# Kernel tuning notes

Hardware: AMD Instinct MI355X
Metric: run time of the kernel (lower is better)

Reference implementation:

```python
import jax, jax.numpy as jnp
from jax import lax
import numpy as np

STRIDE = 16
FH, FW, FC = 100, 160, 256
IMG_H, IMG_W = FH * STRIDE, FW * STRIDE
MIN_SIZE = 16.0
PRE_NMS, POST_NMS = 6000, 300
NMS_T, OUT_NMS_T, SCORE_T = 0.7, 0.5, 0.5
NC = 21          # classes incl. background
POOL, MPOOL = 7, 14
HID = 1024
MC = 128         # mask head channels


def box_iou(a, b):
    # a: [N,4], b: [M,4] in (x1,y1,x2,y2)
    area_a = (a[:, 2] - a[:, 0]) * (a[:, 3] - a[:, 1])
    area_b = (b[:, 2] - b[:, 0]) * (b[:, 3] - b[:, 1])
    lt = jnp.maximum(a[:, None, :2], b[None, :, :2])
    rb = jnp.minimum(a[:, None, 2:], b[None, :, 2:])
    wh = jnp.clip(rb - lt, 0.0)
    inter = wh[..., 0] * wh[..., 1]
    return inter / (area_a[:, None] + area_b[None, :] - inter + 1e-9)


def greedy_nms(iou, thresh):
    # boxes assumed sorted by score desc; returns boolean keep mask
    n = iou.shape[0]
    idxs = jnp.arange(n)
    def body(i, keep):
        sup = keep[i] & (iou[i] > thresh) & (idxs > i)
        return keep & ~sup
    return lax.fori_loop(0, n, body, jnp.ones((n,), bool))


def decode_boxes(deltas, boxes):
    # deltas [...,4], boxes broadcastable [...,4]
    w = boxes[..., 2] - boxes[..., 0]
    h = boxes[..., 3] - boxes[..., 1]
    cx = boxes[..., 0] + 0.5 * w
    cy = boxes[..., 1] + 0.5 * h
    dx, dy, dw, dh = deltas[..., 0], deltas[..., 1], deltas[..., 2], deltas[..., 3]
    pcx = dx * w + cx
    pcy = dy * h + cy
    pw = w * jnp.exp(jnp.minimum(dw, 4.0))
    ph = h * jnp.exp(jnp.minimum(dh, 4.0))
    return jnp.stack([pcx - 0.5 * pw, pcy - 0.5 * ph, pcx + 0.5 * pw, pcy + 0.5 * ph], axis=-1)


def clip_boxes(b):
    return jnp.stack([
        jnp.clip(b[..., 0], 0.0, IMG_W), jnp.clip(b[..., 1], 0.0, IMG_H),
        jnp.clip(b[..., 2], 0.0, IMG_W), jnp.clip(b[..., 3], 0.0, IMG_H)], axis=-1)


def roi_align(feat, rois, out):
    # feat [C,H,W], rois [R,4] in feature-map coords; 1 bilinear sample per bin center
    C, H, W = feat.shape
    R = rois.shape[0]
    x1, y1, x2, y2 = rois[:, 0], rois[:, 1], rois[:, 2], rois[:, 3]
    bw = (x2 - x1) / out
    bh = (y2 - y1) / out
    ctr = jnp.arange(out, dtype=feat.dtype) + 0.5
    sx = x1[:, None] + ctr[None, :] * bw[:, None] - 0.5   # [R,out]
    sy = y1[:, None] + ctr[None, :] * bh[:, None] - 0.5
    xx = jnp.broadcast_to(sx[:, None, :], (R, out, out))
    yy = jnp.broadcast_to(sy[:, :, None], (R, out, out))
    x0 = jnp.clip(jnp.floor(xx), 0, W - 2)
    y0 = jnp.clip(jnp.floor(yy), 0, H - 2)
    fx = jnp.clip(xx - x0, 0.0, 1.0)
    fy = jnp.clip(yy - y0, 0.0, 1.0)
    x0i, y0i = x0.astype(jnp.int32), y0.astype(jnp.int32)
    v00 = feat[:, y0i, x0i]        # [C,R,out,out]
    v01 = feat[:, y0i, x0i + 1]
    v10 = feat[:, y0i + 1, x0i]
    v11 = feat[:, y0i + 1, x0i + 1]
    o = (v00 * ((1 - fy) * (1 - fx))[None] + v01 * ((1 - fy) * fx)[None]
         + v10 * (fy * (1 - fx))[None] + v11 * (fy * fx)[None])
    return o.transpose(1, 0, 2, 3)  # [R,C,out,out]


def setup_inputs() -> dict:
    key = jax.random.key(0)
    ks = jax.random.split(key, 12)
    A = FH * FW * 9
    features = jax.random.normal(ks[0], (1, FC, FH, FW), jnp.float32)
    rpn_logits = jax.random.normal(ks[1], (A, 2), jnp.float32)
    rpn_deltas = jax.random.normal(ks[2], (A, 4), jnp.float32) * 0.1
    # anchor grid: 3 scales x 3 ratios at every stride-16 cell
    cx = (np.arange(FW) + 0.5) * STRIDE
    cy = (np.arange(FH) + 0.5) * STRIDE
    cyg, cxg = np.meshgrid(cy, cx, indexing='ij')  # [FH,FW]
    ws, hs = [], []
    for s in (64.0, 128.0, 256.0):
        for r in (0.5, 1.0, 2.0):
            ws.append(s * np.sqrt(r)); hs.append(s / np.sqrt(r))
    ws = np.asarray(ws, np.float32); hs = np.asarray(hs, np.float32)
    anc = np.stack([cxg[..., None] - ws / 2, cyg[..., None] - hs / 2,
                    cxg[..., None] + ws / 2, cyg[..., None] + hs / 2], axis=-1)
    anchors = jnp.asarray(anc.reshape(-1, 4), jnp.float32)
    W1 = jax.random.normal(ks[3], (FC * POOL * POOL, HID), jnp.float32) * 0.02
    b1 = jnp.zeros((HID,), jnp.float32)
    Wc = jax.random.normal(ks[4], (HID, NC), jnp.float32) * 0.02
    bc = jnp.zeros((NC,), jnp.float32)
    Wr = jax.random.normal(ks[5], (HID, NC * 4), jnp.float32) * 0.02
    br = jnp.zeros((NC * 4,), jnp.float32)
    mw1 = jax.random.normal(ks[6], (MC, FC, 3, 3), jnp.float32) * 0.02
    mb1 = jnp.zeros((MC,), jnp.float32)
    mwd = jax.random.normal(ks[7], (MC, MC, 2, 2), jnp.float32) * 0.02
    mbd = jnp.zeros((MC,), jnp.float32)
    mwo = jax.random.normal(ks[8], (NC, MC, 1, 1), jnp.float32) * 0.02
    mbo = jnp.zeros((NC,), jnp.float32)
    return dict(features=features, rpn_logits=rpn_logits, rpn_deltas=rpn_deltas,
                anchors=anchors, W1=W1, b1=b1, Wc=Wc, bc=bc, Wr=Wr, br=br,
                mw1=mw1, mb1=mb1, mwd=mwd, mbd=mbd, mwo=mwo, mbo=mbo)


def reference(features, rpn_logits, rpn_deltas, anchors, W1, b1, Wc, bc, Wr, br,
              mw1, mb1, mwd, mbd, mwo, mbo):
    feat = features[0]  # [C,FH,FW]
    # --- RPN proposal stage (detached, as in the torch code) ---
    scores = lax.stop_gradient(jax.nn.softmax(rpn_logits, axis=1)[:, 1])
    rois_all = clip_boxes(decode_boxes(lax.stop_gradient(rpn_deltas), anchors))
    ok = ((rois_all[:, 2] - rois_all[:, 0]) >= MIN_SIZE) & ((rois_all[:, 3] - rois_all[:, 1]) >= MIN_SIZE)
    scores = jnp.where(ok, scores, -jnp.inf)
    vals, idx = lax.top_k(scores, PRE_NMS)
    boxes = rois_all[idx]
    keep = greedy_nms(box_iou(boxes, boxes), NMS_T)
    v2, i2 = lax.top_k(jnp.where(keep, vals, -jnp.inf), POST_NMS)
    rois = boxes[i2]  # [R,4]
    # --- ROI heads ---
    roi7 = roi_align(feat, rois / STRIDE, POOL)
    roi14 = roi_align(feat, rois / STRIDE, MPOOL)
    R = POST_NMS
    h = jax.nn.relu(roi7.reshape(R, -1) @ W1 + b1)
    cls_logits = h @ Wc + bc                       # [R,NC]
    roi_deltas = (h @ Wr + br).reshape(R, NC, 4)
    dn = ('NCHW', 'OIHW', 'NCHW')
    x = jax.nn.relu(lax.conv_general_dilated(roi14, mw1, (1, 1), ((1, 1), (1, 1)),
                                             dimension_numbers=dn) + mb1[None, :, None, None])
    x = jax.nn.relu(lax.conv_general_dilated(x, mwd, (1, 1), ((1, 1), (1, 1)), lhs_dilation=(2, 2),
                                             dimension_numbers=dn) + mbd[None, :, None, None])
    mask_logits = lax.conv_general_dilated(x, mwo, (1, 1), ((0, 0), (0, 0)),
                                           dimension_numbers=dn) + mbo[None, :, None, None]  # [R,NC,28,28]
    # --- decode per-class boxes, score/size filter, class-agnostic output NMS ---
    pred_boxes = clip_boxes(decode_boxes(roi_deltas, rois[:, None, :]))  # [R,NC,4]
    sc = jax.nn.softmax(cls_logits, axis=1)[:, 1:].reshape(-1)           # drop background
    bx = pred_boxes[:, 1:].reshape(-1, 4)
    ci = jnp.broadcast_to(jnp.arange(1, NC)[None, :], (R, NC - 1)).reshape(-1) - 1
    ml = mask_logits[:, 1:].reshape(-1, 28, 28)
    valid = (sc > SCORE_T) & ((bx[:, 2] - bx[:, 0]) >= 1.0) & ((bx[:, 3] - bx[:, 1]) >= 1.0)
    scm = jnp.where(valid, sc, -jnp.inf)
    n = scm.shape[0]
    dv, order = lax.top_k(scm, n)     # full descending sort
    dbx = bx[order]
    dci = ci[order]
    dml = ml[order]
    k2 = greedy_nms(box_iou(dbx, dbx), OUT_NMS_T) & jnp.isfinite(dv)
    det_scores = jnp.where(k2, dv, 0.0)
    return det_scores, dbx, dci, k2, dml
```

## Files before the change

kernel.cpp:

```cpp
#include <hip/hip_runtime.h>
#include <stdint.h>

#pragma clang fp contract(off)

typedef unsigned int u32;
typedef unsigned short u16;
typedef unsigned long long u64;
typedef float f32x4 __attribute__((ext_vector_type(4)));
typedef u16 u16x8 __attribute__((ext_vector_type(8)));

#define DEV __device__ __forceinline__

DEV float bf2f(u16 u){ union{u32 i; float f;} v; v.i=((u32)u)<<16; return v.f; }
DEV u16 f2bf(float f){ union{float f; u32 i;} v; v.f=f; u32 b=v.i; return (u16)((b + 0x7fffu + ((b>>16)&1u))>>16); }
DEV u32 fkey(float f){ union{float f; u32 i;} v; v.f=f; u32 b=v.i; return (b&0x80000000u)? ~b : (b|0x80000000u); }
DEV float exp_cr(float x){ return (float)exp((double)x); }

DEV void mfma16(f32x4& d, u16x8 a, u16x8 b){
  asm volatile("v_mfma_f32_16x16x32_bf16 %0, %1, %2, %0" : "+v"(d) : "v"(a), "v"(b));
}

DEV void gload_lds16(const void* g, void* l){
  __builtin_amdgcn_global_load_lds((const __attribute__((address_space(1))) unsigned int*)g,
                                   (__attribute__((address_space(3))) unsigned int*)l, 16, 0, 0);
}

DEV u64 rfl64(u64 v){
  return ((u64)__builtin_amdgcn_readfirstlane((u32)(v>>32))<<32) |
         (u64)__builtin_amdgcn_readfirstlane((u32)v);
}

__global__ void k_rpn(const float* __restrict__ logits, const float* __restrict__ deltas,
                      const float* __restrict__ anchors, float* __restrict__ scores,
                      float* __restrict__ rois_all, u32* __restrict__ hist){
  int i=blockIdx.x*256+threadIdx.x;
  if(i>=144000) return;
  float l0=logits[2*i], l1=logits[2*i+1];
  float m=fmaxf(l0,l1);
  float e0=exp_cr(l0-m), e1=exp_cr(l1-m);
  float s=e1/(e0+e1);
  float a0=anchors[4*i],a1=anchors[4*i+1],a2=anchors[4*i+2],a3=anchors[4*i+3];
  float w=a2-a0, hh=a3-a1;
  float cx=a0+0.5f*w, cy=a1+0.5f*hh;
  float dx=deltas[4*i],dy=deltas[4*i+1],dwv=deltas[4*i+2],dhv=deltas[4*i+3];
  float pcx=dx*w+cx, pcy=dy*hh+cy;
  float pw=w*exp_cr(fminf(dwv,4.f)), ph=hh*exp_cr(fminf(dhv,4.f));
  float x1=fminf(fmaxf(pcx-0.5f*pw,0.f),2560.f);
  float y1=fminf(fmaxf(pcy-0.5f*ph,0.f),1600.f);
  float x2=fminf(fmaxf(pcx+0.5f*pw,0.f),2560.f);
  float y2=fminf(fmaxf(pcy+0.5f*ph,0.f),1600.f);
  float4 bb; bb.x=x1;bb.y=y1;bb.z=x2;bb.w=y2;
  *(float4*)(rois_all+4*i)=bb;
  bool ok=(x2-x1>=16.f)&&(y2-y1>=16.f);
  float sc=ok? s : -INFINITY;
  scores[i]=sc;
  if(ok) atomicAdd(&hist[fkey(sc)>>16],1u);
}

__global__ void k_findbin(const u32* __restrict__ hist, u32* __restrict__ cnt){
  __shared__ u32 cs[1024];
  int t=threadIdx.x;
  u32 s=0;
  for(int b=0;b<64;b++) s+=hist[t*64+b];
  cs[t]=s;
  __syncthreads();
  if(t==0){
    u32 acc=0; int tc=1023;
    for(; tc>=0; tc--){ if(acc+cs[tc]>=6000u) break; acc+=cs[tc]; }
    if(tc<0) tc=0;
    u32 B=(u32)tc*64u;
    for(int b=63;b>=0;b--){
      u32 hb=hist[tc*64+b];
      if(acc+hb>=6000u){ B=(u32)(tc*64+b); break; }
      acc+=hb;
    }
    cnt[2]=B;
  }
}

__global__ void k_compact(const float* __restrict__ scores, u32* __restrict__ cnt, u64* __restrict__ keys){
  int i=blockIdx.x*256+threadIdx.x;
  if(i>=144000) return;
  u32 u=fkey(scores[i]);
  if((u>>16) >= cnt[2]){
    u32 pos=atomicAdd(&cnt[0],1u);
    if(pos<8192u) keys[pos]=((u64)u<<32)|(u64)(~(u32)i);
  }
}

template<bool FROMCNT>
__global__ __launch_bounds__(1024) void k_sort8k(const u64* __restrict__ keys, const u32* __restrict__ cnt,
                                                 int n_fixed, u32* __restrict__ out_idx){
  __shared__ u64 K[8192];
  int n = FROMCNT ? (int)cnt[0] : n_fixed;
  if(n>8192) n=8192;
  for(int i=threadIdx.x;i<8192;i+=1024) K[i]=(i<n)? keys[i] : 0ull;
  __syncthreads();
  for(int k=2;k<=8192;k<<=1){
    for(int j=k>>1;j>0;j>>=1){
      for(int t=threadIdx.x;t<8192;t+=1024){
        int p=t^j;
        if(p>t){
          u64 a=K[t], b=K[p];
          bool up=((t&k)==0);
          if((a<b)==up){ K[t]=b; K[p]=a; }
        }
      }
      __syncthreads();
    }
  }
  for(int i=threadIdx.x;i<6000;i+=1024) out_idx[i]=~((u32)K[i]);
}

__global__ void k_gather6k(const u32* __restrict__ selidx, const float* __restrict__ rois_all,
                           float* __restrict__ boxes6k){
  int i=blockIdx.x*256+threadIdx.x;
  if(i>=6000) return;
  u32 g=selidx[i];
  float4 b=*(const float4*)(rois_all+4*g);
  *(float4*)(boxes6k+4*i)=b;
}

template<int TR>
__global__ void k_masks(const float* __restrict__ boxes, const u32* __restrict__ limitPtr, int limitFixed,
                        float thresh, u64* __restrict__ masks){
  int limit = limitPtr? (int)*limitPtr : limitFixed;
  if(limit>6000) limit=6000;
  long total=(long)limit*94;
  int lane=threadIdx.x&63;
  long w0=(long)blockIdx.x*4 + (threadIdx.x>>6);
  long stride=(long)gridDim.x*4;
  for(long w=w0; w<total; w+=stride){
    int row=(int)(w/94), wrd=(int)(w-(long)row*94);
    int j=wrd*64+lane;
    float4 a=*(const float4*)(boxes+4*row);
    bool bit=false;
    if(j<limit && j>row){
      float4 b=*(const float4*)(boxes+4*j);
      float area_a=(a.z-a.x)*(a.w-a.y);
      float area_b=(b.z-b.x)*(b.w-b.y);
      float ltx=fmaxf(a.x,b.x), lty=fmaxf(a.y,b.y);
      float rbx=fminf(a.z,b.z), rby=fminf(a.w,b.w);
      float wv=fmaxf(rbx-ltx,0.f), hv=fmaxf(rby-lty,0.f);
      float inter=wv*hv;
      float iou=inter/(area_a+area_b-inter+1e-9f);
      bit = iou>thresh;
    }
    u64 mword=__ballot(bit);
    if(lane==0){
      if(TR) masks[(size_t)(row>>6)*6016 + (size_t)wrd*64 + (((row&63)+wrd)&63)]=mword;
      else   masks[(size_t)row*94+wrd]=mword;
    }
  }
}

__global__ __launch_bounds__(512) void k_scan1(const u64* __restrict__ masksT, const float* __restrict__ boxes6k,
                                               float* __restrict__ rois300){
  __shared__ __align__(16) u64 stage[3][6144];
  __shared__ u64 remv[94];
  __shared__ u64 keepw[94];
  __shared__ u32 rsel[304];
  int tid=threadIdx.x, lane=tid&63, wvid=tid>>6;
  int w=tid&127, h=tid>>7;
  bool act=(w<94);
  if(tid<94) remv[tid]=0ull;
  const char* mb=(const char*)masksT;
#pragma unroll
  for(int k=0;k<6;k++){
    int ins=wvid+k*8;
    gload_lds16(mb+(size_t)ins*1024+lane*16, (char*)&stage[0][0]+ins*1024);
  }
#pragma unroll
  for(int k=0;k<6;k++){
    int ins=wvid+k*8;
    gload_lds16(mb+48128+(size_t)ins*1024+lane*16, (char*)&stage[1][0]+ins*1024);
  }
  int tot=0;
  for(int c=0;c<94;c++){
    const u64* sb=&stage[c%3][0];
    if(c<93) asm volatile("s_waitcnt vmcnt(6)" ::: "memory");
    else     asm volatile("s_waitcnt vmcnt(0)" ::: "memory");
    asm volatile("s_waitcnt lgkmcnt(0)" ::: "memory");
    __builtin_amdgcn_s_barrier();
    if(c<92){
      const char* src=mb+(size_t)(c+2)*48128;
      char* dst=(char*)&stage[(c+2)%3][0];
#pragma unroll
      for(int k=0;k<6;k++){
        int ins=wvid+k*8;
        gload_lds16(src+(size_t)ins*1024+lane*16, dst+ins*1024);
      }
    }
    if(wvid==0){
      u64 keep=~rfl64(remv[c]);
      if(c==93) keep&=0x0000FFFFFFFFFFFFull;
      u64 dg=sb[(size_t)c*64+((lane+c)&63)];
      u32 dlo=(u32)dg, dhi=(u32)(dg>>32);
      u64 avail=keep;
      while(avail){
        u32 i=__builtin_amdgcn_readfirstlane((u32)__builtin_ctzll(avail));
        u64 row=((u64)__builtin_amdgcn_readlane(dhi,i)<<32)|(u64)__builtin_amdgcn_readlane(dlo,i);
        keep&=~row;
        avail&=~row;
        avail&=avail-1ull;
      }
      if(lane==0) keepw[c]=keep;
    }
    asm volatile("s_waitcnt lgkmcnt(0)" ::: "memory");
    __builtin_amdgcn_s_barrier();
    u64 kp=rfl64(keepw[c]);
    if(act){
      u64 racc=0ull;
#pragma unroll
      for(int j2=0;j2<16;j2++){
        int r=h*16+j2;
        u64 v=sb[(size_t)w*64+((r+w)&63)];
        racc|=v&((u64)0-((kp>>r)&1ull));
      }
      if(racc) atomicOr(&remv[w],racc);
    }
    tot+=(int)__popcll(kp);
    if(tot>=300) break;
  }
  asm volatile("s_waitcnt vmcnt(0) lgkmcnt(0)" ::: "memory");
  __builtin_amdgcn_s_barrier();
  if(tid==0){
    int cntk=0;
    for(int c=0;c<94&&cntk<300;c++){
      u64 kw=keepw[c];
      while(kw&&cntk<300){ int b=__builtin_ctzll(kw); rsel[cntk++]=(u32)(c*64+b); kw&=kw-1; }
    }
    for(int c=0;c<94&&cntk<300;c++){
      u64 kw=~keepw[c];
      if(c==93) kw&=0x0000FFFFFFFFFFFFull;
      while(kw&&cntk<300){ int b=__builtin_ctzll(kw); rsel[cntk++]=(u32)(c*64+b); kw&=kw-1; }
    }
  }
  __builtin_amdgcn_s_barrier();
  for(int s2=tid;s2<300;s2+=512){
    u32 g=rsel[s2];
    float4 b=*(const float4*)(boxes6k+4*g);
    *(float4*)(rois300+4*s2)=b;
  }
}

__global__ __launch_bounds__(64) void k_scan2(const u64* __restrict__ masks, const u32* __restrict__ cnt,
                                              const float* __restrict__ dv, float* __restrict__ out){
  int lane=threadIdx.x;
  int V=(int)cnt[1]; if(V>6000)V=6000;
  bool ld=lane<47;
  const u64* mrow=masks+lane*2;
  u64 r0=0,r1=0;
  for(int i=0;i<V;i++){
    int w=i>>6;
    u64 v0=__shfl(r0,w>>1);
    u64 v1=__shfl(r1,w>>1);
    u64 word=(w&1)?v1:v0;
    if(!((word>>(i&63))&1ull)){
      if(ld){ r0|=mrow[(size_t)i*94]; r1|=mrow[(size_t)i*94+1]; }
    }
  }
  __shared__ u64 rem[94];
  if(ld){ rem[2*lane]=r0; rem[2*lane+1]=r1; }
  __syncthreads();
  for(int i=lane;i<6000;i+=64){
    bool kept=(i<V)&&!((rem[i>>6]>>(i&63))&1ull);
    out[i]=kept? dv[i]:0.0f;
    out[36000+i]=kept?1.0f:0.0f;
  }
}

__global__ void k_featT(const float* __restrict__ feat, u16* __restrict__ featT){
  __shared__ float tile[32][65];
  int p0=blockIdx.x*64, c0=blockIdx.y*32;
  int t=threadIdx.x;
  int pp=t&63, cc=t>>6;
#pragma unroll
  for(int s=0;s<8;s++)
    tile[cc+s*4][pp]=feat[(size_t)(c0+cc+s*4)*16000+p0+pp];
  __syncthreads();
  int cw=t&31, pw=t>>5;
#pragma unroll
  for(int s=0;s<8;s++)
    featT[(size_t)(p0+pw+s*8)*256+c0+cw]=f2bf(tile[cw][pw+s*8]);
}

template<int OUT>
__global__ void k_roialign(const float* __restrict__ rois, const u16* __restrict__ featT,
                           u16* __restrict__ outbuf){
  int wid=threadIdx.x>>6, lane=threadIdx.x&63;
  int gw=blockIdx.x*4+wid;
  if(gw>=300*OUT*OUT) return;
  int r=gw/(OUT*OUT), q=gw-r*(OUT*OUT), py=q/OUT, px=q-py*OUT;
  float x1=rois[4*r]*0.0625f;
  float y1=rois[4*r+1]*0.0625f;
  float x2=rois[4*r+2]*0.0625f;
  float y2=rois[4*r+3]*0.0625f;
  float bw=(x2-x1)/(float)OUT, bh=(y2-y1)/(float)OUT;
  float xx=x1+((float)px+0.5f)*bw-0.5f;
  float yy=y1+((float)py+0.5f)*bh-0.5f;
  float x0f=fminf(fmaxf(floorf(xx),0.f),158.f);
  float y0f=fminf(fmaxf(floorf(yy),0.f),98.f);
  float fx=fminf(fmaxf(xx-x0f,0.f),1.f);
  float fy=fminf(fmaxf(yy-y0f,0.f),1.f);
  int x0=(int)x0f, y0=(int)y0f;
  float w00=(1.f-fy)*(1.f-fx), w01=(1.f-fy)*fx, w10=fy*(1.f-fx), w11=fy*fx;
  const u16* p00=featT+((size_t)(y0*160+x0))*256+lane*4;
  ushort4 u00=*(const ushort4*)p00;
  ushort4 u01=*(const ushort4*)(p00+256);
  ushort4 u10=*(const ushort4*)(p00+40960);
  ushort4 u11=*(const ushort4*)(p00+41216);
  ushort4 o;
  o.x=f2bf(((bf2f(u00.x)*w00+bf2f(u01.x)*w01)+bf2f(u10.x)*w10)+bf2f(u11.x)*w11);
  o.y=f2bf(((bf2f(u00.y)*w00+bf2f(u01.y)*w01)+bf2f(u10.y)*w10)+bf2f(u11.y)*w11);
  o.z=f2bf(((bf2f(u00.z)*w00+bf2f(u01.z)*w01)+bf2f(u10.z)*w10)+bf2f(u11.z)*w11);
  o.w=f2bf(((bf2f(u00.w)*w00+bf2f(u01.w)*w01)+bf2f(u10.w)*w10)+bf2f(u11.w)*w11);
  *(ushort4*)(outbuf+(size_t)gw*256+lane*4)=o;
}

__global__ void k_prep(const float* __restrict__ mw1, const float* __restrict__ mwd,
                       const float* __restrict__ Wc, const float* __restrict__ Wr,
                       u16* __restrict__ Bc1, u16* __restrict__ B3t, float* __restrict__ WT){
  int i=blockIdx.x*256+threadIdx.x;
  if(i<294912){
    int o=i/2304, rem=i-o*2304, c=rem/9, t=rem-(rem/9)*9;
    Bc1[((size_t)t*256+c)*128+o]=f2bf(mw1[i]);
  }
  if(i<65536){
    int co=i>>9, ci=(i>>2)&127, ky=(i>>1)&1, kxx=i&1;
    int z=ky*2+kxx;
    B3t[((size_t)z*128+co)*128+ci]=f2bf(mwd[i]);
  }
  if(i<107520){
    int j=i>>10, k=i&1023;
    WT[(size_t)j*1024+k]=(j<21)? Wc[(size_t)k*21+j] : Wr[(size_t)k*84+(j-21)];
  }
}

__global__ __launch_bounds__(256) void k_fc1b(const u16* __restrict__ roi7, const float* __restrict__ W1,
                                              float* __restrict__ hp){
  __shared__ u16 Bsm[2][64][72];
  int ks=blockIdx.x, bn=blockIdx.y;
  int kbase=ks*896, n0=bn*64;
  int tid=threadIdx.x, lane=tid&63, wid=tid>>6;
  int wr=wid>>1, wc=wid&1;
  f32x4 acc[5][2][2]={};
  auto stageB=[&](int it,int buf){
    int r=tid>>2, cs=(tid&3)*16;
    int kg=kbase+it*64+r;
    int p=kg>>8, c=kg&255;
    const float* src=W1+(size_t)(c*49+p)*1024+n0+cs;
    float fv[16];
    *(float4*)(fv+0)=((const float4*)src)[0];
    *(float4*)(fv+4)=((const float4*)src)[1];
    *(float4*)(fv+8)=((const float4*)src)[2];
    *(float4*)(fv+12)=((const float4*)src)[3];
#pragma unroll
    for(int ii=0;ii<16;ii++) Bsm[buf][cs+ii][r]=f2bf(fv[ii]);
  };
  stageB(0,0);
  __syncthreads();
  int buf=0;
  for(int it=0;it<14;it++){
    int kk=kbase+it*64;
    u16x8 bfr[2][2];
#pragma unroll
    for(int ks2=0;ks2<2;ks2++){
      int kb=ks2*32+(lane>>4)*8;
#pragma unroll
      for(int fn=0;fn<2;fn++)
        bfr[ks2][fn]=*(const u16x8*)&Bsm[buf][wc*32+fn*16+(lane&15)][kb];
    }
    if(it<13) stageB(it+1,buf^1);
#pragma unroll
    for(int ks2=0;ks2<2;ks2++){
      int kb=ks2*32+(lane>>4)*8;
#pragma unroll
      for(int mt=0;mt<5;mt++){
#pragma unroll
        for(int fm=0;fm<2;fm++){
          int m=mt*64+wr*32+fm*16+(lane&15);
          u16x8 av={0,0,0,0,0,0,0,0};
          if(m<300) av=*(const u16x8*)(roi7+(size_t)m*12544+kk+kb);
          mfma16(acc[mt][fm][0],av,bfr[ks2][0]);
          mfma16(acc[mt][fm][1],av,bfr[ks2][1]);
        }
      }
    }
    __syncthreads();
    buf^=1;
  }
  asm volatile("s_nop 7\ns_nop 7");
  size_t base=((size_t)(ks*16+bn))*300*64;
#pragma unroll
  for(int mt=0;mt<5;mt++)
#pragma unroll
  for(int fm=0;fm<2;fm++)
#pragma unroll
  for(int fn=0;fn<2;fn++){
    int col=wc*32+fn*16+(lane&15);
#pragma unroll
    for(int j=0;j<4;j++){
      int row=mt*64+wr*32+fm*16+(lane>>4)*4+j;
      if(row<300) hp[base+(size_t)row*64+col]=acc[mt][fm][fn][j];
    }
  }
}

__global__ void k_fc1red(const float* __restrict__ hp, const float* __restrict__ b1,
                         float* __restrict__ h){
  int i=blockIdx.x*256+threadIdx.x;
  if(i>=300*1024) return;
  int r=i>>10, n=i&1023;
  int bn=n>>6, c64=n&63;
  float s=b1[n];
#pragma unroll
  for(int ks=0;ks<14;ks++)
    s+=hp[((size_t)(ks*16+bn)*300+r)*64+c64];
  h[(size_t)r*1024+n]=fmaxf(s,0.f);
}

__global__ __launch_bounds__(256) void k_conv1(const u16* __restrict__ roi14, const u16* __restrict__ Bc1,
                                               const float* __restrict__ mb1, u16* __restrict__ x1){
  __shared__ u16 Asm[64][48];
  __shared__ u16 Bsm[128][48];
  __shared__ int rowinf[64];
  int m0=blockIdx.x*64;
  int tid=threadIdx.x, lane=tid&63, wid=tid>>6;
  int wr=wid>>1, wc=wid&1;
  if(tid<64){
    int p=m0+tid;
    if(p<58800){ int r=p/196, q=p-r*196, y=q/14, x=q-y*14; rowinf[tid]=(r<<8)|(y<<4)|x; }
    else rowinf[tid]=-1;
  }
  __syncthreads();
  f32x4 acc[2][4]={};
  for(int it=0; it<72; ++it){
    int kg=it*32;
    int tap=kg>>8, c0=kg&255;
    int ky=tap/3, kx=tap-ky*3;
    {
      int ri=tid>>2, cl=(tid&3)*8;
      int rb=rowinf[ri];
      u16x8 v={0,0,0,0,0,0,0,0};
      if(rb>=0){
        int rr=rb>>8, y=(rb>>4)&15, x=rb&15;
        int yy=y+ky-1, xx=x+kx-1;
        if(yy>=0&&yy<14&&xx>=0&&xx<14)
          v=*(const u16x8*)(roi14+((size_t)((rr*14+yy)*14+xx))*256+c0+cl);
      }
      *(u16x8*)&Asm[ri][cl]=v;
    }
    {
      int kr=tid&31, cs2=(tid>>5)*16;
      const u16x8* s=(const u16x8*)(Bc1+(size_t)(kg+kr)*128+cs2);
      u16x8 v0=s[0], v1=s[1];
#pragma unroll
      for(int ii=0;ii<8;ii++){ Bsm[cs2+ii][kr]=v0[ii]; Bsm[cs2+8+ii][kr]=v1[ii]; }
    }
    __syncthreads();
    int kb=(lane>>4)*8;
    u16x8 a0=*(const u16x8*)&Asm[wr*32+(lane&15)][kb];
    u16x8 a1=*(const u16x8*)&Asm[wr*32+16+(lane&15)][kb];
#pragma unroll
    for(int fn=0;fn<4;fn++){
      u16x8 bv=*(const u16x8*)&Bsm[wc*64+fn*16+(lane&15)][kb];
      mfma16(acc[0][fn],a0,bv);
      mfma16(acc[1][fn],a1,bv);
    }
    __syncthreads();
  }
  asm volatile("s_nop 7\ns_nop 7");
#pragma unroll
  for(int fm=0;fm<2;fm++)
#pragma unroll
  for(int fn=0;fn<4;fn++){
    int col=wc*64+fn*16+(lane&15);
    float bias=mb1[col];
#pragma unroll
    for(int j=0;j<4;j++){
      int row=wr*32+fm*16+(lane>>4)*4+j;
      int p=m0+row;
      if(p<58800) x1[(size_t)p*128+col]=f2bf(fmaxf(acc[fm][fn][j]+bias,0.f));
    }
  }
}

__global__ __launch_bounds__(256) void k_conv2f(const u16* __restrict__ x1, const u16* __restrict__ B3t,
                                                const float* __restrict__ mbd, const float* __restrict__ mwo,
                                                const float* __restrict__ mbo, float* __restrict__ m3){
  __shared__ u16 Asm[64][48];
  __shared__ u16 Bsm[128][48];
  __shared__ u16 X2[64][144];
  __shared__ u16 B4[32][144];
  int m0=blockIdx.x*64, z=blockIdx.y;
  int ky=z>>1, kx=z&1;
  int tid=threadIdx.x, lane=tid&63, wid=tid>>6;
  int wr=wid>>1, wc=wid&1;
  for(int i=tid;i<32*128;i+=256){
    int n=i>>7, k=i&127;
    B4[n][k]=(n<21)? f2bf(mwo[n*128+k]) : (u16)0;
  }
  f32x4 acc[2][4]={};
  for(int it=0;it<4;it++){
    int c0=it*32;
    {
      int ri=tid>>2, cl=(tid&3)*8;
      int p=m0+ri;
      u16x8 v={0,0,0,0,0,0,0,0};
      if(p<58800) v=*(const u16x8*)(x1+(size_t)p*128+c0+cl);
      *(u16x8*)&Asm[ri][cl]=v;
    }
    {
      int n=tid>>1, hf=tid&1;
      const u16x8* s=(const u16x8*)(B3t+((size_t)z*128+n)*128+c0+hf*16);
      u16x8 v0=s[0], v1=s[1];
      *(u16x8*)&Bsm[n][hf*16]=v0;
      *(u16x8*)&Bsm[n][hf*16+8]=v1;
    }
    __syncthreads();
    int kb=(lane>>4)*8;
    u16x8 a0=*(const u16x8*)&Asm[wr*32+(lane&15)][kb];
    u16x8 a1=*(const u16x8*)&Asm[wr*32+16+(lane&15)][kb];
#pragma unroll
    for(int fn=0;fn<4;fn++){
      u16x8 bv=*(const u16x8*)&Bsm[wc*64+fn*16+(lane&15)][kb];
      mfma16(acc[0][fn],a0,bv);
      mfma16(acc[1][fn],a1,bv);
    }
    __syncthreads();
  }
  asm volatile("s_nop 7\ns_nop 7");
#pragma unroll
  for(int fm=0;fm<2;fm++)
#pragma unroll
  for(int fn=0;fn<4;fn++){
    int col=wc*64+fn*16+(lane&15);
    float bias=mbd[col];
#pragma unroll
    for(int j=0;j<4;j++){
      int row=wr*32+fm*16+(lane>>4)*4+j;
      X2[row][col]=f2bf(fmaxf(acc[fm][fn][j]+bias,0.f));
    }
  }
  __syncthreads();
  f32x4 acc2[2]={};
#pragma unroll
  for(int ks=0;ks<4;ks++){
    int kb=ks*32+(lane>>4)*8;
    u16x8 a=*(const u16x8*)&X2[wid*16+(lane&15)][kb];
    u16x8 b0=*(const u16x8*)&B4[(lane&15)][kb];
    u16x8 b1v=*(const u16x8*)&B4[16+(lane&15)][kb];
    mfma16(acc2[0],a,b0);
    mfma16(acc2[1],a,b1v);
  }
  asm volatile("s_nop 7\ns_nop 7");
#pragma unroll
  for(int fn=0;fn<2;fn++){
    int n=fn*16+(lane&15);
    if(n<21){
      float bias=mbo[n];
#pragma unroll
      for(int j=0;j<4;j++){
        int row=wid*16+(lane>>4)*4+j;
        int p=m0+row;
        if(p<58800){
          int r=p/196, q=p-r*196, iy=q/14, ix=q-iy*14;
          int oy=2*iy+(1-ky), ox=2*ix+(1-kx);
          m3[((size_t)r*21+n)*784 + oy*28+ox]=acc2[fn][j]+bias;
        }
      }
    }
  }
}

__global__ void k_head(const float* __restrict__ h, const float* __restrict__ WT,
                       const float* __restrict__ bc, const float* __restrict__ br,
                       const float* __restrict__ rois300, float* __restrict__ bxb,
                       float* __restrict__ scm, u64* __restrict__ keys2, u32* __restrict__ cnt){
  __shared__ float hs[1024];
  __shared__ float lg[105];
  __shared__ float scs[21];
  int r=blockIdx.x, t=threadIdx.x;
  for(int i=t;i<1024;i+=256) hs[i]=h[(size_t)r*1024+i];
  __syncthreads();
  if(t<105){
    const float* wrow=WT+(size_t)t*1024;
    float s=0.f;
    for(int k=0;k<1024;k+=4){
      float4 wv=*(const float4*)(wrow+k);
      s+=hs[k]*wv.x; s+=hs[k+1]*wv.y; s+=hs[k+2]*wv.z; s+=hs[k+3]*wv.w;
    }
    lg[t]=s+((t<21)?bc[t]:br[t-21]);
  }
  __syncthreads();
  if(t==0){
    float m=lg[0];
    for(int c=1;c<21;c++) m=fmaxf(m,lg[c]);
    float sum=0.f;
    for(int c=0;c<21;c++){ float e=exp_cr(lg[c]-m); scs[c]=e; sum+=e; }
    for(int c=0;c<21;c++) scs[c]=scs[c]/sum;
  }
  __syncthreads();
  if(t<20){
    int c=t+1;
    float rx1=rois300[4*r],ry1=rois300[4*r+1],rx2=rois300[4*r+2],ry2=rois300[4*r+3];
    float w=rx2-rx1, hh=ry2-ry1;
    float cx=rx1+0.5f*w, cy=ry1+0.5f*hh;
    float dx=lg[21+c*4+0], dy=lg[21+c*4+1], dwv=lg[21+c*4+2], dhv=lg[21+c*4+3];
    float pcx=dx*w+cx, pcy=dy*hh+cy;
    float pw=w*exp_cr(fminf(dwv,4.f)), ph=hh*exp_cr(fminf(dhv,4.f));
    float bx1=fminf(fmaxf(pcx-0.5f*pw,0.f),2560.f);
    float by1=fminf(fmaxf(pcy-0.5f*ph,0.f),1600.f);
    float bx2=fminf(fmaxf(pcx+0.5f*pw,0.f),2560.f);
    float by2=fminf(fmaxf(pcy+0.5f*ph,0.f),1600.f);
    int e=r*20+t;
    bxb[4*e]=bx1; bxb[4*e+1]=by1; bxb[4*e+2]=bx2; bxb[4*e+3]=by2;
    float sc=scs[c];
    bool valid=(sc>0.5f)&&(bx2-bx1>=1.f)&&(by2-by1>=1.f);
    float sv=valid? sc : -INFINITY;
    scm[e]=sv;
    keys2[e]=((u64)fkey(sv)<<32)|(u64)(~(u32)e);
    if(valid) atomicAdd(&cnt[1],1u);
  }
}

__global__ void k_detprep(const u32* __restrict__ order, const float* __restrict__ scm,
                          const float* __restrict__ bxb, float* __restrict__ dv,
                          float* __restrict__ dbx, float* __restrict__ out){
  int i=blockIdx.x*256+threadIdx.x;
  if(i>=6000) return;
  u32 g=order[i];
  float4 b=*(const float4*)(bxb+4*g);
  *(float4*)(dbx+4*i)=b;
  dv[i]=scm[g];
  *(float4*)(out+6000+4*i)=b;
  out[30000+i]=(float)(g%20u);
}

__global__ void k_dml(const u32* __restrict__ order, const float* __restrict__ m3, float* __restrict__ out){
  int idx=blockIdx.x*256+threadIdx.x;
  if(idx>=4704000) return;
  int e=idx/784, q=idx-e*784;
  u32 g=order[e];
  int r=(int)(g/20u), c=(int)(g%20u)+1;
  out[42000+idx]=m3[((size_t)r*21+c)*784+q];
}

extern "C" void kernel_launch(void* const* d_in, const int* in_sizes, int n_in,
                              void* d_out, int out_size, void* d_ws, size_t ws_size,
                              hipStream_t stream){
  (void)in_sizes; (void)n_in; (void)out_size;
  const float* features =(const float*)d_in[0];
  const float* rpn_logits=(const float*)d_in[1];
  const float* rpn_deltas=(const float*)d_in[2];
  const float* anchors  =(const float*)d_in[3];
  const float* W1=(const float*)d_in[4];
  const float* b1=(const float*)d_in[5];
  const float* Wc=(const float*)d_in[6];
  const float* bc=(const float*)d_in[7];
  const float* Wr=(const float*)d_in[8];
  const float* br=(const float*)d_in[9];
  const float* mw1=(const float*)d_in[10];
  const float* mb1=(const float*)d_in[11];
  const float* mwd=(const float*)d_in[12];
  const float* mbd=(const float*)d_in[13];
  const float* mwo=(const float*)d_in[14];
  const float* mbo=(const float*)d_in[15];
  float* out=(float*)d_out;

  char* base=(char*)d_ws; size_t off=0;
  auto alloc=[&](size_t bytes)->void*{ off=(off+255)&~(size_t)255; void* p=base+off; off+=bytes; return p; };
  u32* hist     =(u32*)alloc(65536*4);
  u32* cnt      =(u32*)alloc(64);
  float* scores =(float*)alloc(144000*4);
  float* rois_all=(float*)alloc((size_t)144000*16);
  u64* keys1    =(u64*)alloc(8192*8);
  u32* selidx   =(u32*)alloc(6000*4);
  float* boxes6k=(float*)alloc(6000*16);
  u64* masksT   =(u64*)alloc((size_t)94*6016*8 + 1024);
  u64* masks    =(u64*)alloc((size_t)6000*94*8);
  float* rois300=(float*)alloc(300*16);
  u16* featT    =(u16*)alloc((size_t)16000*256*2);
  u16* roi7     =(u16*)alloc((size_t)300*49*256*2);
  u16* roi14    =(u16*)alloc((size_t)300*196*256*2);
  float* hbuf   =(float*)alloc((size_t)300*1024*4);
  float* hp     =(float*)alloc((size_t)224*300*64*4);
  float* WT     =(float*)alloc((size_t)105*1024*4);
  float* bxb    =(float*)alloc(6000*16);
  float* scm    =(float*)alloc(6000*4);
  u64* keys2    =(u64*)alloc(8192*8);
  u32* order    =(u32*)alloc(6000*4);
  float* dv     =(float*)alloc(6000*4);
  float* dbx    =(float*)alloc(6000*16);
  u16* x1       =(u16*)alloc((size_t)58800*128*2);
  u16* Bc1      =(u16*)alloc((size_t)2304*128*2);
  u16* B3t      =(u16*)alloc((size_t)4*128*128*2);
  float* m3     =(float*)alloc((size_t)58800*21*4);
  if(off > ws_size) return;

  hipMemsetAsync(hist,0,65536*4,stream);
  hipMemsetAsync(cnt,0,64,stream);

  k_prep<<<1152,256,0,stream>>>(mw1,mwd,Wc,Wr,Bc1,B3t,WT);
  k_featT<<<dim3(250,8),256,0,stream>>>(features,featT);

  k_rpn<<<563,256,0,stream>>>(rpn_logits,rpn_deltas,anchors,scores,rois_all,hist);
  k_findbin<<<1,1024,0,stream>>>(hist,cnt);
  k_compact<<<563,256,0,stream>>>(scores,cnt,keys1);
  k_sort8k<true><<<1,1024,0,stream>>>(keys1,cnt,0,selidx);
  k_gather6k<<<24,256,0,stream>>>(selidx,rois_all,boxes6k);
  k_masks<1><<<2048,256,0,stream>>>(boxes6k,nullptr,6000,0.7f,masksT);
  k_scan1<<<1,512,0,stream>>>(masksT,boxes6k,rois300);

  k_roialign<7><<<3675,256,0,stream>>>(rois300,featT,roi7);
  k_roialign<14><<<14700,256,0,stream>>>(rois300,featT,roi14);

  k_fc1b<<<dim3(14,16),256,0,stream>>>(roi7,W1,hp);
  k_fc1red<<<1200,256,0,stream>>>(hp,b1,hbuf);
  k_conv1<<<919,256,0,stream>>>(roi14,Bc1,mb1,x1);
  k_conv2f<<<dim3(919,4),256,0,stream>>>(x1,B3t,mbd,mwo,mbo,m3);

  k_head<<<300,256,0,stream>>>(hbuf,WT,bc,br,rois300,bxb,scm,keys2,cnt);
  k_sort8k<false><<<1,1024,0,stream>>>(keys2,nullptr,6000,order);
  k_detprep<<<24,256,0,stream>>>(order,scm,bxb,dv,dbx,out);
  k_masks<0><<<512,256,0,stream>>>(dbx,cnt+1,0,0.5f,masks);
  k_scan2<<<1,64,0,stream>>>(masks,cnt,dv,out);
  k_dml<<<18375,256,0,stream>>>(order,m3,out);
}
```

Baseline: 866.0 us.

## Replace single-block bitonic sorts with histogram bucket sort and rank-count sort

```diff
diff --git a/kernel.cpp b/kernel.cpp
--- a/kernel.cpp
+++ b/kernel.cpp
@@ -57,59 +57,76 @@
   if(ok) atomicAdd(&hist[fkey(sc)>>16],1u);
 }
 
-__global__ void k_findbin(const u32* __restrict__ hist, u32* __restrict__ cnt){
+__global__ __launch_bounds__(1024) void k_findbin(const u32* __restrict__ hist, u32* __restrict__ cnt,
+                                                  u32* __restrict__ base){
   __shared__ u32 cs[1024];
+  __shared__ u32 hb[1024];
   int t=threadIdx.x;
   u32 s=0;
   for(int b=0;b<64;b++) s+=hist[t*64+b];
   cs[t]=s;
   __syncthreads();
   if(t==0){
-    u32 acc=0; int tc=1023;
+    u32 acc=0;
+    for(int i=1023;i>=0;i--){ hb[i]=acc; acc+=cs[i]; }
+    acc=0; int tc=1023;
     for(; tc>=0; tc--){ if(acc+cs[tc]>=6000u) break; acc+=cs[tc]; }
     if(tc<0) tc=0;
     u32 B=(u32)tc*64u;
     for(int b=63;b>=0;b--){
-      u32 hb=hist[tc*64+b];
-      if(acc+hb>=6000u){ B=(u32)(tc*64+b); break; }
-      acc+=hb;
+      u32 hbv=hist[tc*64+b];
+      if(acc+hbv>=6000u){ B=(u32)(tc*64+b); break; }
+      acc+=hbv;
     }
     cnt[2]=B;
   }
-}
-
-__global__ void k_compact(const float* __restrict__ scores, u32* __restrict__ cnt, u64* __restrict__ keys){
+  __syncthreads();
+  u32 run=hb[t];
+  for(int b=63;b>=0;b--){ base[t*64+b]=run; run+=hist[t*64+b]; }
+}
+
+__global__ void k_bucket(const float* __restrict__ scores, const u32* __restrict__ cnt,
+                         const u32* __restrict__ base, u32* __restrict__ cntbin,
+                         u64* __restrict__ bucket){
   int i=blockIdx.x*256+threadIdx.x;
   if(i>=144000) return;
   u32 u=fkey(scores[i]);
-  if((u>>16) >= cnt[2]){
-    u32 pos=atomicAdd(&cnt[0],1u);
-    if(pos<8192u) keys[pos]=((u64)u<<32)|(u64)(~(u32)i);
-  }
-}
-
-template<bool FROMCNT>
-__global__ __launch_bounds__(1024) void k_sort8k(const u64* __restrict__ keys, const u32* __restrict__ cnt,
-                                                 int n_fixed, u32* __restrict__ out_idx){
-  __shared__ u64 K[8192];
-  int n = FROMCNT ? (int)cnt[0] : n_fixed;
-  if(n>8192) n=8192;
-  for(int i=threadIdx.x;i<8192;i+=1024) K[i]=(i<n)? keys[i] : 0ull;
-  __syncthreads();
-  for(int k=2;k<=8192;k<<=1){
-    for(int j=k>>1;j>0;j>>=1){
-      for(int t=threadIdx.x;t<8192;t+=1024){
-        int p=t^j;
-        if(p>t){
-          u64 a=K[t], b=K[p];
-          bool up=((t&k)==0);
-          if((a<b)==up){ K[t]=b; K[p]=a; }
-        }
-      }
+  u32 bin=u>>16;
+  if(bin>=cnt[2]){
+    u32 pos=base[bin]+atomicAdd(&cntbin[bin],1u);
+    if(pos<8192u) bucket[pos]=((u64)u<<32)|(u64)(~(u32)i);
+  }
+}
+
+__global__ __launch_bounds__(256) void k_binsort(const u32* __restrict__ cnt, const u32* __restrict__ base,
+                                                 const u32* __restrict__ hist, const u64* __restrict__ bucket,
+                                                 u32* __restrict__ selidx){
+  __shared__ u64 SL[4096];
+  u32 B=cnt[2];
+  for(u32 bin=B+blockIdx.x; bin<65536u; bin+=gridDim.x){
+    u32 m=hist[bin];
+    if(m==0u) continue;
+    u32 bs=base[bin];
+    if(bs>=6000u) continue;
+    if(bs+m>8192u) m=8192u-bs;
+    if(m==1u){ if(threadIdx.x==0) selidx[bs]=~(u32)bucket[bs]; continue; }
+    if(m<=4096u){
+      for(u32 i=threadIdx.x;i<m;i+=256) SL[i]=bucket[bs+i];
       __syncthreads();
-    }
-  }
-  for(int i=threadIdx.x;i<6000;i+=1024) out_idx[i]=~((u32)K[i]);
+      for(u32 i=threadIdx.x;i<m;i+=256){
+        u64 k=SL[i]; u32 r=0;
+        for(u32 j=0;j<m;j++) r+=(SL[j]>k);
+        if(bs+r<6000u) selidx[bs+r]=~(u32)k;
+      }
+      __syncthreads();
+    } else {
+      for(u32 i=threadIdx.x;i<m;i+=256){
+        u64 k=bucket[bs+i]; u32 r=0;
+        for(u32 j=0;j<m;j++) r+=(bucket[bs+j]>k);
+        if(bs+r<6000u) selidx[bs+r]=~(u32)k;
+      }
+    }
+  }
 }
 
 __global__ void k_gather6k(const u32* __restrict__ selidx, const float* __restrict__ rois_all,
@@ -577,7 +594,7 @@
 __global__ void k_head(const float* __restrict__ h, const float* __restrict__ WT,
                        const float* __restrict__ bc, const float* __restrict__ br,
                        const float* __restrict__ rois300, float* __restrict__ bxb,
-                       float* __restrict__ scm, u64* __restrict__ keys2, u32* __restrict__ cnt){
+                       float* __restrict__ scm, u32* __restrict__ cnt){
   __shared__ float hs[1024];
   __shared__ float lg[105];
   __shared__ float scs[21];
@@ -620,8 +637,42 @@
     bool valid=(sc>0.5f)&&(bx2-bx1>=1.f)&&(by2-by1>=1.f);
     float sv=valid? sc : -INFINITY;
     scm[e]=sv;
-    keys2[e]=((u64)fkey(sv)<<32)|(u64)(~(u32)e);
     if(valid) atomicAdd(&cnt[1],1u);
+  }
+}
+
+__global__ __launch_bounds__(1024) void k_detsort(const float* __restrict__ scm, u32* __restrict__ order){
+  __shared__ float ss[6000];
+  __shared__ u32 tp[1025];
+  int t=threadIdx.x;
+  for(int i=t;i<6000;i+=1024) ss[i]=scm[i];
+  __syncthreads();
+  int e0=t*6, e1=e0+6; if(e1>6000) e1=6000; if(e0>6000) e0=6000;
+  u32 c=0;
+  for(int e=e0;e<e1;e++) c+=(ss[e]!=-INFINITY);
+  tp[t]=c;
+  __syncthreads();
+  if(t==0){
+    u32 run=0;
+    for(int i=0;i<1024;i++){ u32 cc=tp[i]; tp[i]=run; run+=cc; }
+    tp[1024]=run;
+  }
+  __syncthreads();
+  u32 V=tp[1024];
+  u32 pv=tp[t];
+  for(int e=e0;e<e1;e++){
+    float se=ss[e];
+    if(se!=-INFINITY){
+      u32 r=0;
+      for(int j=0;j<6000;j++){
+        float sj=ss[j];
+        r+=(sj>se)||((sj==se)&&(j<e));
+      }
+      order[r]=(u32)e;
+      pv++;
+    } else {
+      order[V+(u32)e-pv]=(u32)e;
+    }
   }
 }
 
@@ -669,13 +720,15 @@
   const float* mbo=(const float*)d_in[15];
   float* out=(float*)d_out;
 
-  char* base=(char*)d_ws; size_t off=0;
-  auto alloc=[&](size_t bytes)->void*{ off=(off+255)&~(size_t)255; void* p=base+off; off+=bytes; return p; };
+  char* base_=(char*)d_ws; size_t off=0;
+  auto alloc=[&](size_t bytes)->void*{ off=(off+255)&~(size_t)255; void* p=base_+off; off+=bytes; return p; };
   u32* hist     =(u32*)alloc(65536*4);
+  u32* binbase  =(u32*)alloc(65536*4);
+  u32* cntbin   =(u32*)alloc(65536*4);
   u32* cnt      =(u32*)alloc(64);
   float* scores =(float*)alloc(144000*4);
   float* rois_all=(float*)alloc((size_t)144000*16);
-  u64* keys1    =(u64*)alloc(8192*8);
+  u64* bucket   =(u64*)alloc(8192*8);
   u32* selidx   =(u32*)alloc(6000*4);
   float* boxes6k=(float*)alloc(6000*16);
   u64* masksT   =(u64*)alloc((size_t)94*6016*8 + 1024);
@@ -689,7 +742,6 @@
   float* WT     =(float*)alloc((size_t)105*1024*4);
   float* bxb    =(float*)alloc(6000*16);
   float* scm    =(float*)alloc(6000*4);
-  u64* keys2    =(u64*)alloc(8192*8);
   u32* order    =(u32*)alloc(6000*4);
   float* dv     =(float*)alloc(6000*4);
   float* dbx    =(float*)alloc(6000*16);
@@ -700,15 +752,16 @@
   if(off > ws_size) return;
 
   hipMemsetAsync(hist,0,65536*4,stream);
+  hipMemsetAsync(cntbin,0,65536*4,stream);
   hipMemsetAsync(cnt,0,64,stream);
 
   k_prep<<<1152,256,0,stream>>>(mw1,mwd,Wc,Wr,Bc1,B3t,WT);
   k_featT<<<dim3(250,8),256,0,stream>>>(features,featT);
 
   k_rpn<<<563,256,0,stream>>>(rpn_logits,rpn_deltas,anchors,scores,rois_all,hist);
-  k_findbin<<<1,1024,0,stream>>>(hist,cnt);
-  k_compact<<<563,256,0,stream>>>(scores,cnt,keys1);
-  k_sort8k<true><<<1,1024,0,stream>>>(keys1,cnt,0,selidx);
+  k_findbin<<<1,1024,0,stream>>>(hist,cnt,binbase);
+  k_bucket<<<563,256,0,stream>>>(scores,cnt,binbase,cntbin,bucket);
+  k_binsort<<<2048,256,0,stream>>>(cnt,binbase,hist,bucket,selidx);
   k_gather6k<<<24,256,0,stream>>>(selidx,rois_all,boxes6k);
   k_masks<1><<<2048,256,0,stream>>>(boxes6k,nullptr,6000,0.7f,masksT);
   k_scan1<<<1,512,0,stream>>>(masksT,boxes6k,rois300);
@@ -721,8 +774,8 @@
   k_conv1<<<919,256,0,stream>>>(roi14,Bc1,mb1,x1);
   k_conv2f<<<dim3(919,4),256,0,stream>>>(x1,B3t,mbd,mwo,mbo,m3);
 
-  k_head<<<300,256,0,stream>>>(hbuf,WT,bc,br,rois300,bxb,scm,keys2,cnt);
-  k_sort8k<false><<<1,1024,0,stream>>>(keys2,nullptr,6000,order);
+  k_head<<<300,256,0,stream>>>(hbuf,WT,bc,br,rois300,bxb,scm,cnt);
+  k_detsort<<<1,1024,0,stream>>>(scm,order);
   k_detprep<<<24,256,0,stream>>>(order,scm,bxb,dv,dbx,out);
   k_masks<0><<<512,256,0,stream>>>(dbx,cnt+1,0,0.5f,masks);
   k_scan2<<<1,64,0,stream>>>(masks,cnt,dv,out);
```

Result: faster. 732.2 us (-15.4%).
